# Kernel tuning notes

Measured on AMD Instinct MI355X. Metric: run time of the kernel, lower is better.

## Reference

```python
import math
import jax, jax.numpy as jnp
import numpy as np

T_STEPS = 128       # number of diffusion 'experts'
BASE = 64
CH = BASE * 2       # 128 working channels
TE = 256            # time embedding dim
B, IN_C, H, W = 8, 3, 128, 128
EPS = 1e-5


def _conv(x, w, b):
    # x: [N,C,H,W], w: [O,I,3,3] (or 1x1)
    y = jax.lax.conv_general_dilated(x, w, (1, 1), 'SAME',
                                     dimension_numbers=('NCHW', 'OIHW', 'NCHW'))
    return y + b[None, :, None, None]


def _gn(x, scale, bias, groups=8):
    n, c, h, w = x.shape
    xg = x.reshape(n, groups, c // groups, h, w)
    m = xg.mean((2, 3, 4), keepdims=True)
    v = xg.var((2, 3, 4), keepdims=True)
    xn = ((xg - m) * jax.lax.rsqrt(v + EPS)).reshape(n, c, h, w)
    return xn * scale[None, :, None, None] + bias[None, :, None, None]


def setup_inputs() -> dict:
    key = jax.random.key(0)
    ks = iter(jax.random.split(key, 64))
    def p(shape, s=0.05):
        return jax.random.normal(next(ks), shape, jnp.float32) * s
    return {
        'x': jax.random.normal(next(ks), (B, IN_C, H, W), jnp.float32),
        't': jax.random.randint(next(ks), (B,), 0, T_STEPS),
        # feature_extraction
        'fe_w1': p((BASE, IN_C, 3, 3)), 'fe_b1': jnp.zeros((BASE,), jnp.float32),
        'fe_g1s': jnp.ones((BASE,), jnp.float32), 'fe_g1b': jnp.zeros((BASE,), jnp.float32),
        'fe_w2': p((CH, BASE, 3, 3)), 'fe_b2': jnp.zeros((CH,), jnp.float32),
        'fe_g2s': jnp.ones((CH,), jnp.float32), 'fe_g2b': jnp.zeros((CH,), jnp.float32),
        # stacked per-step expert params [T, ...]
        'mlp_w1': p((T_STEPS, TE, TE)), 'mlp_b1': jnp.zeros((T_STEPS, TE), jnp.float32),
        'mlp_w2': p((T_STEPS, CH, TE)), 'mlp_b2': jnp.zeros((T_STEPS, CH), jnp.float32),
        'c1w': p((T_STEPS, CH, CH + 1, 3, 3)), 'c1b': jnp.zeros((T_STEPS, CH), jnp.float32),
        'g1s': jnp.ones((T_STEPS, CH), jnp.float32), 'g1b': jnp.zeros((T_STEPS, CH), jnp.float32),
        'c2w': p((T_STEPS, CH, CH, 3, 3)), 'c2b': jnp.zeros((T_STEPS, CH), jnp.float32),
        'g2s': jnp.ones((T_STEPS, CH), jnp.float32), 'g2b': jnp.zeros((T_STEPS, CH), jnp.float32),
        'c3w': p((T_STEPS, CH, CH, 3, 3)), 'c3b': jnp.zeros((T_STEPS, CH), jnp.float32),
        # color_reconstruction
        'cr_w1': p((BASE, CH, 3, 3)), 'cr_b1': jnp.zeros((BASE,), jnp.float32),
        'cr_gs': jnp.ones((BASE,), jnp.float32), 'cr_gb': jnp.zeros((BASE,), jnp.float32),
        'cr_w2': p((IN_C, BASE, 3, 3)), 'cr_b2': jnp.zeros((IN_C,), jnp.float32),
        # weight_generator (1x1 conv on pooled features)
        'wg_w': p((1, CH, 1, 1)), 'wg_b': jnp.zeros((1,), jnp.float32),
    }


def _expert(xi, tei, w1, b1, w2, b2, cw1, cb1, gs1, gb1, cw2, cb2, gs2, gb2, cw3, cb3):
    # Single-sample DiffusionStep. xi: [C,H,W], tei: [TE]
    h = jax.nn.silu(w1 @ tei + b1)
    tc = (w2 @ h + b2).mean()  # scalar time channel (fix of original view(-1,1,1,1) bug)
    xb = xi[None]  # [1,C,H,W]
    tmap = jnp.broadcast_to(tc, (1, 1) + xi.shape[1:])
    z = jnp.concatenate([xb, tmap], axis=1)  # [1,C+1,H,W]
    z = jax.nn.silu(_gn(_conv(z, cw1, cb1), gs1, gb1))
    z = jax.nn.silu(_gn(_conv(z, cw2, cb2), gs2, gb2))
    z = _conv(z, cw3, cb3)
    return z[0]


def _forward(x, t, fe_w1, fe_b1, fe_g1s, fe_g1b, fe_w2, fe_b2, fe_g2s, fe_g2b,
             mlp_w1, mlp_b1, mlp_w2, mlp_b2, c1w, c1b, g1s, g1b,
             c2w, c2b, g2s, g2b, c3w, c3b,
             cr_w1, cr_b1, cr_gs, cr_gb, cr_w2, cr_b2, wg_w, wg_b):
    feat = jax.nn.silu(_gn(_conv(x, fe_w1, fe_b1), fe_g1s, fe_g1b))
    feat = jax.nn.silu(_gn(_conv(feat, fe_w2, fe_b2), fe_g2s, fe_g2b))  # [B,CH,H,W]

    # sinusoidal time embedding
    half = TE // 2
    freqs = jnp.exp(jnp.arange(half, dtype=jnp.float32) * (-math.log(10000.0) / (half - 1)))
    e = t.astype(jnp.float32)[:, None] * freqs[None, :]
    temb = jnp.concatenate([jnp.sin(e), jnp.cos(e)], axis=-1)  # [B,TE]

    # Each sample matches exactly one step: gather its expert weights, apply once.
    g = lambda a: jnp.take(a, t, axis=0)
    noise = jax.vmap(_expert)(feat, temb,
                              g(mlp_w1), g(mlp_b1), g(mlp_w2), g(mlp_b2),
                              g(c1w), g(c1b), g(g1s), g(g1b),
                              g(c2w), g(c2b), g(g2s), g(g2b),
                              g(c3w), g(c3b))
    alpha = 1.0 - t.astype(jnp.float32) / T_STEPS
    x_t = feat - alpha[:, None, None, None] * noise

    r = jax.nn.silu(_gn(_conv(x_t, cr_w1, cr_b1), cr_gs, cr_gb))
    restored = jax.nn.sigmoid(_conv(r, cr_w2, cr_b2))  # [B,3,H,W]

    pooled = x_t.mean((2, 3))  # adaptive avg pool to 1x1 -> [B,CH]
    weight = jax.nn.sigmoid(pooled @ wg_w[:, :, 0, 0].T + wg_b)[:, :, None, None]  # [B,1,1,1]
    return restored, weight


def reference(x, t, fe_w1, fe_b1, fe_g1s, fe_g1b, fe_w2, fe_b2, fe_g2s, fe_g2b,
              mlp_w1, mlp_b1, mlp_w2, mlp_b2, c1w, c1b, g1s, g1b,
              c2w, c2b, g2s, g2b, c3w, c3b,
              cr_w1, cr_b1, cr_gs, cr_gb, cr_w2, cr_b2, wg_w, wg_b):
    return _forward(x, t, fe_w1, fe_b1, fe_g1s, fe_g1b, fe_w2, fe_b2, fe_g2s, fe_g2b,
                    mlp_w1, mlp_b1, mlp_w2, mlp_b2, c1w, c1b, g1s, g1b,
                    c2w, c2b, g2s, g2b, c3w, c3b,
                    cr_w1, cr_b1, cr_gs, cr_gb, cr_w2, cr_b2, wg_w, wg_b)
```

## Files before the change

### kernel.cpp

```cpp
#include <hip/hip_runtime.h>
#include <hip/hip_bf16.h>

typedef __hip_bfloat16 bf16;

#define HW 128
#define IMG 16384
#define EPSV 1e-5f

typedef __bf16 b16x8 __attribute__((ext_vector_type(8)));
typedef float f32x16 __attribute__((ext_vector_type(16)));

__device__ __forceinline__ float u2f(unsigned int u){ union{unsigned int i; float f;}c; c.i=u; return c.f; }
__device__ __forceinline__ float blo(unsigned int u){ return u2f(u<<16); }
__device__ __forceinline__ float bhi(unsigned int u){ return u2f(u & 0xffff0000u); }
__device__ __forceinline__ unsigned short f2bu(float v){ bf16 h=__float2bfloat16(v); union{bf16 b; unsigned short s;}c; c.b=h; return c.s; }
__device__ __forceinline__ unsigned int pk(float a, float b){ return (unsigned int)f2bu(a) | ((unsigned int)f2bu(b)<<16); }
__device__ __forceinline__ bf16 f2b(float v){ return __float2bfloat16(v); }
__device__ __forceinline__ float sigm(float x){ return 1.f/(1.f+__expf(-x)); }

__device__ __forceinline__ void gload16(const void* g, void* l) {
    __builtin_amdgcn_global_load_lds((const __attribute__((address_space(1))) unsigned int*)(g),
                                     (__attribute__((address_space(3))) unsigned int*)(l), 16, 0, 0);
}

__device__ __forceinline__ f32x16 MFMA(b16x8 a, b16x8 b, f32x16 c){
    return __builtin_amdgcn_mfma_f32_32x32x16_bf16(a, b, c, 0, 0, 0);
}

template<int CIN, int COUT, bool TADD, bool FUSE_GN, bool FUSE_XT>
__global__ void __launch_bounds__(256, 2)
mfma_conv3x3(const bf16* __restrict__ act,
             const bf16* __restrict__ Wt,
             const float* __restrict__ Bt,
             bf16* __restrict__ outp,
             const float* __restrict__ Tt,
             const bf16* __restrict__ zerobuf,
             float* __restrict__ gpart,
             const bf16* __restrict__ featA,
             const int* __restrict__ tsel,
             const float* __restrict__ wgw,
             float* __restrict__ wpart)
{
    static_assert(CIN==64 || CIN==128, "");
    static_assert(COUT==64 || COUT==128, "");
    constexpr int NT  = COUT/64;
    constexpr int CH  = CIN/64;
    constexpr int P   = 9*CH;
    constexpr int WCH = COUT/8;
    constexpr int WSZ = WCH*1024;

    __shared__ char Xb[33792];
    __shared__ char Wa[2][WSZ];
    __shared__ float redS[4][4], redSS[4][4], redW[4];

    const int n    = blockIdx.z;
    const int tile = blockIdx.x;
    const int y0   = tile*2;
    const int tid  = threadIdx.x;
    const int lane = tid & 63;
    const int wid  = tid >> 6;
    const int wm   = wid >> 1;
    const int wn   = wid & 1;
    const int l31  = lane & 31;
    const int lhi  = lane >> 5;

    const bf16* actN = act + (size_t)n * IMG * CIN;
    const bf16* WtN  = Wt  + (size_t)n * 9 * COUT * CIN;

    f32x16 acc[4][NT];
    #pragma unroll
    for (int i=0;i<4;++i)
        #pragma unroll
        for (int j=0;j<NT;++j)
            #pragma unroll
            for (int k=0;k<16;++k) acc[i][j][k] = 0.f;

    auto stage_X = [&](int dy, int ch) {
        const int ry0 = y0 + dy - 1;
        for (int u = wid; u < 33; u += 4) {
            int s = u*8 + (lane>>3);
            int g = lane & 7;
            int r  = (s >= 130) ? 1 : 0;
            int xp = s - r*130;
            int xx = xp - 1;
            int ry = ry0 + r;
            const void* src = zerobuf;
            if (s < 260 && (unsigned)xx < 128u && (unsigned)ry < 128u)
                src = actN + ((size_t)(ry*128 + xx)*CIN + ch*64 + 8*(g ^ (s&7)));
            gload16(src, Xb + u*1024);
        }
    };
    auto stage_W = [&](int r, int ch, int buf) {
        for (int u = wid; u < WCH; u += 4) {
            int co = u*8 + (lane>>3);
            int g  = lane & 7;
            const void* src = WtN + ((size_t)(r*COUT + co)*CIN + ch*64 + 8*(g ^ (co&7)));
            gload16(src, Wa[buf] + u*1024);
        }
    };

    stage_X(0, 0);
    stage_W(0, 0, 0);
    __syncthreads();

    int buf = 0;
    for (int p = 0; p < P; ++p) {
        const int dx = p % 3;
        const int pc = p / 3;
        const int ch = pc % CH;
        const int dy = pc / CH;
        const bool last = (p+1 == P);

        if (!last) {
            const int pn  = p + 1;
            const int ndx = pn % 3;
            const int npc = pn / 3;
            const int nch = npc % CH;
            const int ndy = npc / CH;
            stage_W(ndy*3 + ndx, nch, buf ^ 1);
        }
        (void)dy; (void)ch;

        __builtin_amdgcn_s_setprio(1);
        #pragma unroll
        for (int s = 0; s < 4; ++s) {
            const int koff = s*32 + lhi*16;
            b16x8 bfr[NT];
            #pragma unroll
            for (int q = 0; q < NT; ++q) {
                int co = wn*32*NT + q*32 + l31;
                bfr[q] = *(const b16x8*)(Wa[buf] + co*128 + (koff ^ ((co&7)<<4)));
            }
            b16x8 afr[4];
            #pragma unroll
            for (int mt = 0; mt < 4; ++mt) {
                int sl = wm*130 + mt*32 + l31 + dx;
                afr[mt] = *(const b16x8*)(Xb + sl*128 + (koff ^ ((sl&7)<<4)));
            }
            #pragma unroll
            for (int mt = 0; mt < 4; ++mt)
                #pragma unroll
                for (int q = 0; q < NT; ++q)
                    acc[mt][q] = MFMA(afr[mt], bfr[q], acc[mt][q]);
        }
        __builtin_amdgcn_s_setprio(0);

        if (!last) {
            if (dx == 2) {
                __syncthreads();
                const int pn  = p + 1;
                const int npc = pn / 3;
                stage_X(npc / CH, npc % CH);
                __syncthreads();
            } else {
                __syncthreads();
            }
        }
        buf ^= 1;
    }

    const float* BtN = Bt + n*COUT;
    const int y = y0 + wm;
    bf16* outRow = outp + ((size_t)n*IMG + (size_t)y*128)*COUT;
    const bf16* featRow = FUSE_XT ? (featA + ((size_t)n*IMG + (size_t)y*128)*COUT) : nullptr;
    float alpha = 0.f;
    if (FUSE_XT) alpha = 1.f - (float)tsel[n] * (1.f/128.f);

    float gs[NT], gss[NT], wsum = 0.f;
    #pragma unroll
    for (int q = 0; q < NT; ++q) { gs[q]=0.f; gss[q]=0.f; }

    #pragma unroll
    for (int q = 0; q < NT; ++q) {
        const int co = wn*32*NT + q*32 + l31;
        const float bv = BtN[co];
        float wg = 0.f;
        if (FUSE_XT) wg = wgw[co];
        float T0=0.f, T1=0.f, T2=0.f;
        if (TADD) {
            int yt = (y==0) ? 0 : (y==127 ? 2 : 1);
            const float* Tp = Tt + (size_t)(n*COUT + co)*9 + yt*3;
            T0 = Tp[0]; T1 = Tp[1]; T2 = Tp[2];
        }
        #pragma unroll
        for (int mt = 0; mt < 4; ++mt) {
            #pragma unroll
            for (int reg = 0; reg < 16; ++reg) {
                const int x = mt*32 + (reg&3) + 8*(reg>>2) + 4*lhi;
                float v = acc[mt][q][reg] + bv;
                if (TADD) v += (x==0) ? T0 : (x==127 ? T2 : T1);
                if (FUSE_GN) { gs[q] += v; gss[q] += v*v; }
                if (FUSE_XT) {
                    float fv = __bfloat162float(featRow[(size_t)x*COUT + co]);
                    float xt = fv - alpha*v;
                    outRow[(size_t)x*COUT + co] = f2b(xt);
                    wsum += xt * wg;
                } else {
                    outRow[(size_t)x*COUT + co] = f2b(v);
                }
            }
        }
    }

    if (FUSE_GN) {
        constexpr int LG = (COUT==128) ? 4 : 3;
        #pragma unroll
        for (int q = 0; q < NT; ++q) {
            float a = gs[q], b = gss[q];
            #pragma unroll
            for (int m = 1; m < (1<<LG); m <<= 1) { a += __shfl_xor(a, m); b += __shfl_xor(b, m); }
            a += __shfl_xor(a, 32); b += __shfl_xor(b, 32);
            const int co = wn*32*NT + q*32 + l31;
            if (lhi == 0 && (l31 & ((1<<LG)-1)) == 0) {
                int j = (co >> LG) & 3;
                redS[wid][j] = a; redSS[wid][j] = b;
            }
        }
        __syncthreads();
        if (tid < 8) {
            int g = tid, wn_ = g>>2, j = g&3;
            float S  = redS[wn_][j]  + redS[2+wn_][j];
            float SS = redSS[wn_][j] + redSS[2+wn_][j];
            gpart[((size_t)(n*64 + tile))*16 + 2*g]     = S;
            gpart[((size_t)(n*64 + tile))*16 + 2*g + 1] = SS;
        }
    }
    if (FUSE_XT) {
        float a = wsum;
        #pragma unroll
        for (int m = 1; m < 64; m <<= 1) a += __shfl_xor(a, m);
        if (lane == 0) redW[wid] = a;
        __syncthreads();
        if (tid == 0) wpart[n*64 + tile] = redW[0]+redW[1]+redW[2]+redW[3];
    }
}

__global__ void __launch_bounds__(256)
wtprep_kernel(const float* __restrict__ w, const float* __restrict__ b,
              const int* __restrict__ t, bf16* __restrict__ Wt, float* __restrict__ Bt,
              int CO, int COsrc, int CIN, int CINW, int gather)
{
    int idx = blockIdx.x*256 + threadIdx.x;
    int total = 8*9*CO*CIN;
    if (idx >= total) return;
    int cin = idx & (CIN-1);
    int tmp = idx / CIN;
    int co  = tmp % CO;
    int tmp2 = tmp / CO;
    int r   = tmp2 % 9;
    int n   = tmp2 / 9;
    int sel = gather ? t[n] : 0;
    float v = 0.f;
    if (co < COsrc) v = w[(((size_t)sel*COsrc + co)*CINW + cin)*9 + r];
    Wt[idx] = f2b(v);
    if (cin==0 && r==0) Bt[n*CO+co] = (co < COsrc) ? b[(size_t)sel*COsrc + co] : 0.f;
}

__global__ void __launch_bounds__(256)
tprep_kernel(const int* __restrict__ t, const float* __restrict__ c1w,
             const float* __restrict__ tc, float* __restrict__ Tt)
{
    int idx = blockIdx.x*256 + threadIdx.x;
    if (idx >= 8*128) return;
    int n = idx >> 7, co = idx & 127;
    const float* wp = c1w + ((size_t)t[n]*128 + co)*129*9 + 128*9;
    float w9[9];
    #pragma unroll
    for (int i=0;i<9;++i) w9[i] = wp[i];
    float tcv = tc[n];
    #pragma unroll
    for (int yt=0; yt<3; ++yt)
        #pragma unroll
        for (int xt=0; xt<3; ++xt) {
            float s = 0.f;
            #pragma unroll
            for (int dy=0; dy<3; ++dy)
                #pragma unroll
                for (int dx=0; dx<3; ++dx) {
                    bool vy = (yt==0) ? (dy>=1) : ((yt==2) ? (dy<=1) : true);
                    bool vx = (xt==0) ? (dx>=1) : ((xt==2) ? (dx<=1) : true);
                    if (vy && vx) s += w9[dy*3+dx];
                }
            Tt[(size_t)idx*9 + yt*3+xt] = tcv*s;
        }
}

__global__ void __launch_bounds__(256)
fe1_kernel(const float* __restrict__ in, const float* __restrict__ w,
           const float* __restrict__ bias, bf16* __restrict__ out)
{
    const int n   = blockIdx.z;
    const int co0 = blockIdx.y * 8;
    const int tx0 = (blockIdx.x & 7) * 16;
    const int ty0 = (blockIdx.x >> 3) * 16;
    const int lx = threadIdx.x & 15, ly = threadIdx.x >> 4;
    __shared__ float tileS[18][19];
    float acc[8];
    #pragma unroll
    for (int i=0;i<8;++i) acc[i] = bias[co0+i];
    const float* inN = in + (size_t)n*3*IMG;
    for (int ci=0; ci<3; ++ci) {
        __syncthreads();
        for (int idx = threadIdx.x; idx < 18*18; idx += 256) {
            int tyy = idx/18, txx = idx - tyy*18;
            int gy = ty0+tyy-1, gx = tx0+txx-1;
            float v = 0.f;
            if ((unsigned)gy < 128u && (unsigned)gx < 128u) v = inN[ci*IMG + gy*128+gx];
            tileS[tyy][txx] = v;
        }
        __syncthreads();
        float v[9];
        #pragma unroll
        for (int ky=0;ky<3;++ky)
            #pragma unroll
            for (int kx=0;kx<3;++kx) v[ky*3+kx] = tileS[ly+ky][lx+kx];
        #pragma unroll
        for (int c=0;c<8;++c) {
            const float* wp = w + ((co0+c)*3 + ci)*9;
            #pragma unroll
            for (int k=0;k<9;++k) acc[c] = fmaf(v[k], wp[k], acc[c]);
        }
    }
    int gy = ty0+ly, gx = tx0+lx;
    uint4 o; o.x = pk(acc[0],acc[1]); o.y = pk(acc[2],acc[3]);
    o.z = pk(acc[4],acc[5]); o.w = pk(acc[6],acc[7]);
    *(uint4*)(out + ((size_t)n*IMG + gy*128+gx)*64 + co0) = o;
}

template<int C>
__global__ void __launch_bounds__(256)
gn_stats_nhwc(const bf16* __restrict__ x, float* __restrict__ partials)
{
    constexpr int L2CPG = (C==128) ? 4 : 3;
    const int chunk = blockIdx.x, n = blockIdx.y;
    const int t = threadIdx.x;
    const uint4* pv = (const uint4*)(x + ((size_t)n*IMG + chunk*256 + t)*C);
    float s[8], ss[8];
    #pragma unroll
    for (int g=0; g<8; ++g) { s[g]=0.f; ss[g]=0.f; }
    #pragma unroll
    for (int v=0; v<C/8; ++v) {
        int g = (v*8) >> L2CPG;
        uint4 u = pv[v];
        float f0=blo(u.x), f1=bhi(u.x), f2=blo(u.y), f3=bhi(u.y);
        float f4=blo(u.z), f5=bhi(u.z), f6=blo(u.w), f7=bhi(u.w);
        s[g]  += ((f0+f1)+(f2+f3)) + ((f4+f5)+(f6+f7));
        ss[g] += ((f0*f0+f1*f1)+(f2*f2+f3*f3)) + ((f4*f4+f5*f5)+(f6*f6+f7*f7));
    }
    __shared__ float sh[16][256];
    #pragma unroll
    for (int g=0; g<8; ++g) { sh[2*g][t] = s[g]; sh[2*g+1][t] = ss[g]; }
    __syncthreads();
    for (int off=128; off>0; off>>=1) {
        if (t < off) {
            #pragma unroll
            for (int k=0;k<16;++k) sh[k][t] += sh[k][t+off];
        }
        __syncthreads();
    }
    if (t < 16) partials[((size_t)n*64 + chunk)*16 + t] = sh[t][0];
}

__global__ void __launch_bounds__(128)
gn_final(const float* __restrict__ partials, const float* __restrict__ scale,
         const float* __restrict__ bias, const int* __restrict__ tsel,
         int C, int l2cpg, float* __restrict__ scA, float* __restrict__ biA)
{
    int n = blockIdx.x, c = threadIdx.x;
    if (c >= C) return;
    int g = c >> l2cpg;
    float s=0.f, ss=0.f;
    for (int k=0;k<64;++k) {
        s  += partials[((size_t)n*64+k)*16 + 2*g];
        ss += partials[((size_t)n*64+k)*16 + 2*g + 1];
    }
    float cnt = (float)IMG * (float)(C>>3);
    float m = s/cnt, var = ss/cnt - m*m;
    float r = rsqrtf(var + EPSV);
    int po = tsel ? tsel[n]*C : 0;
    float sc = scale[po+c]*r;
    scA[n*C+c] = sc;
    biA[n*C+c] = bias[po+c] - m*sc;
}

template<int C>
__global__ void __launch_bounds__(256)
gn_apply_nhwc(bf16* __restrict__ x, const float* __restrict__ scA, const float* __restrict__ biA)
{
    size_t e0 = ((size_t)blockIdx.x*256 + threadIdx.x)*8;
    int n = (int)(e0 >> ((C==128) ? 21 : 20));
    int c0 = (int)(e0 & (C-1));
    const float4 sA = *(const float4*)(scA + n*C + c0);
    const float4 sB = *(const float4*)(scA + n*C + c0 + 4);
    const float4 bA = *(const float4*)(biA + n*C + c0);
    const float4 bB = *(const float4*)(biA + n*C + c0 + 4);
    uint4* p = (uint4*)(x + e0);
    uint4 u = *p;
    float f[8] = {blo(u.x),bhi(u.x),blo(u.y),bhi(u.y),blo(u.z),bhi(u.z),blo(u.w),bhi(u.w)};
    f[0]=f[0]*sA.x+bA.x; f[1]=f[1]*sA.y+bA.y; f[2]=f[2]*sA.z+bA.z; f[3]=f[3]*sA.w+bA.w;
    f[4]=f[4]*sB.x+bB.x; f[5]=f[5]*sB.y+bB.y; f[6]=f[6]*sB.z+bB.z; f[7]=f[7]*sB.w+bB.w;
    #pragma unroll
    for (int i=0;i<8;++i) f[i] = f[i]*sigm(f[i]);
    u.x = pk(f[0],f[1]); u.y = pk(f[2],f[3]); u.z = pk(f[4],f[5]); u.w = pk(f[6],f[7]);
    *p = u;
}

__global__ void __launch_bounds__(256)
time_mlp_kernel(const int* __restrict__ t,
                const float* __restrict__ w1, const float* __restrict__ b1,
                const float* __restrict__ w2, const float* __restrict__ b2,
                float* __restrict__ tc)
{
    const int n = blockIdx.x;
    const int ti = t[n];
    const int tid = threadIdx.x;
    __shared__ float temb[256];
    __shared__ float h[256];
    {
        int j = tid & 127;
        float fr = expf(-9.210340371976184f / 127.f * (float)j);
        float e = (float)ti * fr;
        temb[tid] = (tid < 128) ? sinf(e) : cosf(e);
    }
    __syncthreads();
    {
        const float* w1p = w1 + ((size_t)ti * 256 + tid) * 256;
        float s = b1[(size_t)ti * 256 + tid];
        for (int j = 0; j < 256; ++j) s += w1p[j] * temb[j];
        h[tid] = s * sigm(s);
    }
    __syncthreads();
    float part = 0.f;
    if (tid < 128) {
        const float* w2p = w2 + ((size_t)ti * 128 + tid) * 256;
        float s = b2[(size_t)ti * 128 + tid];
        for (int j = 0; j < 256; ++j) s += w2p[j] * h[j];
        part = s;
    }
    __shared__ float red[256];
    red[tid] = part;
    __syncthreads();
    for (int off = 128; off > 0; off >>= 1) {
        if (tid < off) red[tid] += red[tid + off];
        __syncthreads();
    }
    if (tid == 0) tc[n] = red[0] * (1.f / 128.f);
}

__global__ void __launch_bounds__(64)
weight_final_kernel(const float* __restrict__ wpart, const float* __restrict__ wg_b,
                    float* __restrict__ outw)
{
    const int n = blockIdx.x;
    float s = wpart[n*64 + threadIdx.x];
    #pragma unroll
    for (int m = 1; m < 64; m <<= 1) s += __shfl_xor(s, m);
    if (threadIdx.x == 0) outw[n] = sigm(s * (1.f/16384.f) + wg_b[0]);
}

__global__ void __launch_bounds__(256)
extract_kernel(const bf16* __restrict__ in, float* __restrict__ out)
{
    int n = blockIdx.y;
    int px = blockIdx.x*256 + threadIdx.x;
    const bf16* p = in + ((size_t)n*IMG + px)*64;
    float r0 = __bfloat162float(p[0]);
    float r1 = __bfloat162float(p[1]);
    float r2 = __bfloat162float(p[2]);
    size_t ob = (size_t)n*3*IMG + px;
    out[ob]         = sigm(r0);
    out[ob + IMG]   = sigm(r1);
    out[ob + 2*IMG] = sigm(r2);
}

extern "C" void kernel_launch(void* const* d_in, const int* in_sizes, int n_in,
                              void* d_out, int out_size, void* d_ws, size_t ws_size,
                              hipStream_t stream)
{
    (void)in_sizes; (void)n_in; (void)out_size; (void)ws_size;

    const float* x      = (const float*)d_in[0];
    const int*   t      = (const int*)  d_in[1];
    const float* fe_w1  = (const float*)d_in[2];
    const float* fe_b1  = (const float*)d_in[3];
    const float* fe_g1s = (const float*)d_in[4];
    const float* fe_g1b = (const float*)d_in[5];
    const float* fe_w2  = (const float*)d_in[6];
    const float* fe_b2  = (const float*)d_in[7];
    const float* fe_g2s = (const float*)d_in[8];
    const float* fe_g2b = (const float*)d_in[9];
    const float* mlp_w1 = (const float*)d_in[10];
    const float* mlp_b1 = (const float*)d_in[11];
    const float* mlp_w2 = (const float*)d_in[12];
    const float* mlp_b2 = (const float*)d_in[13];
    const float* c1w    = (const float*)d_in[14];
    const float* c1b    = (const float*)d_in[15];
    const float* g1s    = (const float*)d_in[16];
    const float* g1b    = (const float*)d_in[17];
    const float* c2w    = (const float*)d_in[18];
    const float* c2b    = (const float*)d_in[19];
    const float* g2s    = (const float*)d_in[20];
    const float* g2b    = (const float*)d_in[21];
    const float* c3w    = (const float*)d_in[22];
    const float* c3b    = (const float*)d_in[23];
    const float* cr_w1  = (const float*)d_in[24];
    const float* cr_b1  = (const float*)d_in[25];
    const float* cr_gs  = (const float*)d_in[26];
    const float* cr_gb  = (const float*)d_in[27];
    const float* cr_w2  = (const float*)d_in[28];
    const float* cr_b2  = (const float*)d_in[29];
    const float* wg_w   = (const float*)d_in[30];
    const float* wg_b   = (const float*)d_in[31];

    char* ws = (char*)d_ws;
    bf16* A   = (bf16*)(ws);
    bf16* Bb  = (bf16*)(ws + 33554432);
    bf16* Cb  = (bf16*)(ws + 67108864);
    bf16* Wt  = (bf16*)(ws + 100663296);
    float* Bt = (float*)(ws + 103022592);
    float* Tt = (float*)(ws + 103026688);
    float* tc = (float*)(ws + 103063552);
    bf16* zb  = (bf16*)(ws + 103063616);
    float* gp = (float*)(ws + 103063680);
    float* scA = (float*)(ws + 103096448);
    float* biA = (float*)(ws + 103100544);
    float* wp  = (float*)(ws + 103104640);

    float* out_img = (float*)d_out;
    float* out_w   = out_img + 393216;

    dim3 blk(256);
    dim3 cgrid(64, 1, 8);
    hipMemsetAsync(zb, 0, 64, stream);

    time_mlp_kernel<<<8, blk, 0, stream>>>(t, mlp_w1, mlp_b1, mlp_w2, mlp_b2, tc);
    tprep_kernel<<<4, blk, 0, stream>>>(t, c1w, tc, Tt);

    fe1_kernel<<<dim3(64, 8, 8), blk, 0, stream>>>(x, fe_w1, fe_b1, Bb);
    gn_stats_nhwc<64><<<dim3(64, 8), blk, 0, stream>>>(Bb, gp);
    gn_final<<<8, 128, 0, stream>>>(gp, fe_g1s, fe_g1b, nullptr, 64, 3, scA, biA);
    gn_apply_nhwc<64><<<4096, blk, 0, stream>>>(Bb, scA, biA);

    wtprep_kernel<<<2304, blk, 0, stream>>>(fe_w2, fe_b2, t, Wt, Bt, 128, 128, 64, 64, 0);
    mfma_conv3x3<64,128,false,true,false><<<cgrid, blk, 0, stream>>>(Bb, Wt, Bt, A, nullptr, zb, gp, nullptr, nullptr, nullptr, nullptr);
    gn_final<<<8, 128, 0, stream>>>(gp, fe_g2s, fe_g2b, nullptr, 128, 4, scA, biA);
    gn_apply_nhwc<128><<<8192, blk, 0, stream>>>(A, scA, biA);

    wtprep_kernel<<<4608, blk, 0, stream>>>(c1w, c1b, t, Wt, Bt, 128, 128, 128, 129, 1);
    mfma_conv3x3<128,128,true,true,false><<<cgrid, blk, 0, stream>>>(A, Wt, Bt, Bb, Tt, zb, gp, nullptr, nullptr, nullptr, nullptr);
    gn_final<<<8, 128, 0, stream>>>(gp, g1s, g1b, t, 128, 4, scA, biA);
    gn_apply_nhwc<128><<<8192, blk, 0, stream>>>(Bb, scA, biA);

    wtprep_kernel<<<4608, blk, 0, stream>>>(c2w, c2b, t, Wt, Bt, 128, 128, 128, 128, 1);
    mfma_conv3x3<128,128,false,true,false><<<cgrid, blk, 0, stream>>>(Bb, Wt, Bt, Cb, nullptr, zb, gp, nullptr, nullptr, nullptr, nullptr);
    gn_final<<<8, 128, 0, stream>>>(gp, g2s, g2b, t, 128, 4, scA, biA);
    gn_apply_nhwc<128><<<8192, blk, 0, stream>>>(Cb, scA, biA);

    wtprep_kernel<<<4608, blk, 0, stream>>>(c3w, c3b, t, Wt, Bt, 128, 128, 128, 128, 1);
    mfma_conv3x3<128,128,false,false,true><<<cgrid, blk, 0, stream>>>(Cb, Wt, Bt, Bb, nullptr, zb, nullptr, A, t, wg_w, wp);
    weight_final_kernel<<<8, 64, 0, stream>>>(wp, wg_b, out_w);

    wtprep_kernel<<<2304, blk, 0, stream>>>(cr_w1, cr_b1, t, Wt, Bt, 64, 64, 128, 128, 0);
    mfma_conv3x3<128,64,false,true,false><<<cgrid, blk, 0, stream>>>(Bb, Wt, Bt, Cb, nullptr, zb, gp, nullptr, nullptr, nullptr, nullptr);
    gn_final<<<8, 128, 0, stream>>>(gp, cr_gs, cr_gb, nullptr, 64, 3, scA, biA);
    gn_apply_nhwc<64><<<4096, blk, 0, stream>>>(Cb, scA, biA);

    wtprep_kernel<<<1152, blk, 0, stream>>>(cr_w2, cr_b2, t, Wt, Bt, 64, 3, 64, 64, 0);
    mfma_conv3x3<64,64,false,false,false><<<cgrid, blk, 0, stream>>>(Cb, Wt, Bt, A, nullptr, zb, nullptr, nullptr, nullptr, nullptr, nullptr);
    extract_kernel<<<dim3(64, 8), blk, 0, stream>>>(A, out_img);
}
```

Measured before the change: 375.7 us.

## Use two waves per conv block, each computing all output channels

The conv kernel drops from 4 waves (2x2 split over rows and channels) to 2 waves, one per output row. Each wave now computes every output channel, so its accumulator tile doubles and it reuses each A fragment across all channel tiles. This cuts LDS reads per MFMA but doubles per-thread accumulator registers and halves the threads available for staging and latency hiding. The GroupNorm partial-sum reduction and the weight reduction are rewritten for the new wave layout.

```diff
diff --git a/kernel.cpp b/kernel.cpp
--- a/kernel.cpp
+++ b/kernel.cpp
@@ -28,7 +28,7 @@
 }
 
 template<int CIN, int COUT, bool TADD, bool FUSE_GN, bool FUSE_XT>
-__global__ void __launch_bounds__(256, 2)
+__global__ void __launch_bounds__(128, 1)
 mfma_conv3x3(const bf16* __restrict__ act,
              const bf16* __restrict__ Wt,
              const float* __restrict__ Bt,
@@ -43,7 +43,7 @@
 {
     static_assert(CIN==64 || CIN==128, "");
     static_assert(COUT==64 || COUT==128, "");
-    constexpr int NT  = COUT/64;
+    constexpr int Q   = COUT/32;
     constexpr int CH  = CIN/64;
     constexpr int P   = 9*CH;
     constexpr int WCH = COUT/8;
@@ -51,7 +51,7 @@
 
     __shared__ char Xb[33792];
     __shared__ char Wa[2][WSZ];
-    __shared__ float redS[4][4], redSS[4][4], redW[4];
+    __shared__ float redS[2][8], redSS[2][8], redW[2];
 
     const int n    = blockIdx.z;
     const int tile = blockIdx.x;
@@ -59,25 +59,24 @@
     const int tid  = threadIdx.x;
     const int lane = tid & 63;
     const int wid  = tid >> 6;
-    const int wm   = wid >> 1;
-    const int wn   = wid & 1;
+    const int wm   = wid;
     const int l31  = lane & 31;
     const int lhi  = lane >> 5;
 
     const bf16* actN = act + (size_t)n * IMG * CIN;
     const bf16* WtN  = Wt  + (size_t)n * 9 * COUT * CIN;
 
-    f32x16 acc[4][NT];
+    f32x16 acc[4][Q];
     #pragma unroll
     for (int i=0;i<4;++i)
         #pragma unroll
-        for (int j=0;j<NT;++j)
+        for (int j=0;j<Q;++j)
             #pragma unroll
             for (int k=0;k<16;++k) acc[i][j][k] = 0.f;
 
     auto stage_X = [&](int dy, int ch) {
         const int ry0 = y0 + dy - 1;
-        for (int u = wid; u < 33; u += 4) {
+        for (int u = wid; u < 33; u += 2) {
             int s = u*8 + (lane>>3);
             int g = lane & 7;
             int r  = (s >= 130) ? 1 : 0;
@@ -91,7 +90,7 @@
         }
     };
     auto stage_W = [&](int r, int ch, int buf) {
-        for (int u = wid; u < WCH; u += 4) {
+        for (int u = wid; u < WCH; u += 2) {
             int co = u*8 + (lane>>3);
             int g  = lane & 7;
             const void* src = WtN + ((size_t)(r*COUT + co)*CIN + ch*64 + 8*(g ^ (co&7)));
@@ -106,9 +105,6 @@
     int buf = 0;
     for (int p = 0; p < P; ++p) {
         const int dx = p % 3;
-        const int pc = p / 3;
-        const int ch = pc % CH;
-        const int dy = pc / CH;
         const bool last = (p+1 == P);
 
         if (!last) {
@@ -119,16 +115,15 @@
             const int ndy = npc / CH;
             stage_W(ndy*3 + ndx, nch, buf ^ 1);
         }
-        (void)dy; (void)ch;
 
         __builtin_amdgcn_s_setprio(1);
         #pragma unroll
         for (int s = 0; s < 4; ++s) {
             const int koff = s*32 + lhi*16;
-            b16x8 bfr[NT];
-            #pragma unroll
-            for (int q = 0; q < NT; ++q) {
-                int co = wn*32*NT + q*32 + l31;
+            b16x8 bfr[Q];
+            #pragma unroll
+            for (int q = 0; q < Q; ++q) {
+                int co = q*32 + l31;
                 bfr[q] = *(const b16x8*)(Wa[buf] + co*128 + (koff ^ ((co&7)<<4)));
             }
             b16x8 afr[4];
@@ -140,7 +135,7 @@
             #pragma unroll
             for (int mt = 0; mt < 4; ++mt)
                 #pragma unroll
-                for (int q = 0; q < NT; ++q)
+                for (int q = 0; q < Q; ++q)
                     acc[mt][q] = MFMA(afr[mt], bfr[q], acc[mt][q]);
         }
         __builtin_amdgcn_s_setprio(0);
@@ -166,13 +161,13 @@
     float alpha = 0.f;
     if (FUSE_XT) alpha = 1.f - (float)tsel[n] * (1.f/128.f);
 
-    float gs[NT], gss[NT], wsum = 0.f;
-    #pragma unroll
-    for (int q = 0; q < NT; ++q) { gs[q]=0.f; gss[q]=0.f; }
-
-    #pragma unroll
-    for (int q = 0; q < NT; ++q) {
-        const int co = wn*32*NT + q*32 + l31;
+    float gs[Q], gss[Q], wsum = 0.f;
+    #pragma unroll
+    for (int q = 0; q < Q; ++q) { gs[q]=0.f; gss[q]=0.f; }
+
+    #pragma unroll
+    for (int q = 0; q < Q; ++q) {
+        const int co = q*32 + l31;
         const float bv = BtN[co];
         float wg = 0.f;
         if (FUSE_XT) wg = wgw[co];
@@ -203,26 +198,26 @@
     }
 
     if (FUSE_GN) {
-        constexpr int LG = (COUT==128) ? 4 : 3;
-        #pragma unroll
-        for (int q = 0; q < NT; ++q) {
+        #pragma unroll
+        for (int q = 0; q < Q; ++q) {
             float a = gs[q], b = gss[q];
-            #pragma unroll
-            for (int m = 1; m < (1<<LG); m <<= 1) { a += __shfl_xor(a, m); b += __shfl_xor(b, m); }
-            a += __shfl_xor(a, 32); b += __shfl_xor(b, 32);
-            const int co = wn*32*NT + q*32 + l31;
-            if (lhi == 0 && (l31 & ((1<<LG)-1)) == 0) {
-                int j = (co >> LG) & 3;
-                redS[wid][j] = a; redSS[wid][j] = b;
+            a += __shfl_xor(a,1);  b += __shfl_xor(b,1);
+            a += __shfl_xor(a,2);  b += __shfl_xor(b,2);
+            a += __shfl_xor(a,4);  b += __shfl_xor(b,4);
+            if (COUT == 128) { a += __shfl_xor(a,8); b += __shfl_xor(b,8); }
+            a += __shfl_xor(a,32); b += __shfl_xor(b,32);
+            if (COUT == 128) {
+                if ((lane & 47) == 0) { int j = q*2 + (l31>>4); redS[wid][j] = a; redSS[wid][j] = b; }
+            } else {
+                if ((lane & 39) == 0) { int j = q*4 + (l31>>3); redS[wid][j] = a; redSS[wid][j] = b; }
             }
         }
         __syncthreads();
         if (tid < 8) {
-            int g = tid, wn_ = g>>2, j = g&3;
-            float S  = redS[wn_][j]  + redS[2+wn_][j];
-            float SS = redSS[wn_][j] + redSS[2+wn_][j];
-            gpart[((size_t)(n*64 + tile))*16 + 2*g]     = S;
-            gpart[((size_t)(n*64 + tile))*16 + 2*g + 1] = SS;
+            float S  = redS[0][tid]  + redS[1][tid];
+            float SS = redSS[0][tid] + redSS[1][tid];
+            gpart[((size_t)(n*64 + tile))*16 + 2*tid]     = S;
+            gpart[((size_t)(n*64 + tile))*16 + 2*tid + 1] = SS;
         }
     }
     if (FUSE_XT) {
@@ -231,7 +226,7 @@
         for (int m = 1; m < 64; m <<= 1) a += __shfl_xor(a, m);
         if (lane == 0) redW[wid] = a;
         __syncthreads();
-        if (tid == 0) wpart[n*64 + tile] = redW[0]+redW[1]+redW[2]+redW[3];
+        if (tid == 0) wpart[n*64 + tile] = redW[0] + redW[1];
     }
 }
 
@@ -530,6 +525,7 @@
     float* out_w   = out_img + 393216;
 
     dim3 blk(256);
+    dim3 cblk(128);
     dim3 cgrid(64, 1, 8);
     hipMemsetAsync(zb, 0, 64, stream);
 
@@ -542,30 +538,30 @@
     gn_apply_nhwc<64><<<4096, blk, 0, stream>>>(Bb, scA, biA);
 
     wtprep_kernel<<<2304, blk, 0, stream>>>(fe_w2, fe_b2, t, Wt, Bt, 128, 128, 64, 64, 0);
-    mfma_conv3x3<64,128,false,true,false><<<cgrid, blk, 0, stream>>>(Bb, Wt, Bt, A, nullptr, zb, gp, nullptr, nullptr, nullptr, nullptr);
+    mfma_conv3x3<64,128,false,true,false><<<cgrid, cblk, 0, stream>>>(Bb, Wt, Bt, A, nullptr, zb, gp, nullptr, nullptr, nullptr, nullptr);
     gn_final<<<8, 128, 0, stream>>>(gp, fe_g2s, fe_g2b, nullptr, 128, 4, scA, biA);
     gn_apply_nhwc<128><<<8192, blk, 0, stream>>>(A, scA, biA);
 
     wtprep_kernel<<<4608, blk, 0, stream>>>(c1w, c1b, t, Wt, Bt, 128, 128, 128, 129, 1);
-    mfma_conv3x3<128,128,true,true,false><<<cgrid, blk, 0, stream>>>(A, Wt, Bt, Bb, Tt, zb, gp, nullptr, nullptr, nullptr, nullptr);
+    mfma_conv3x3<128,128,true,true,false><<<cgrid, cblk, 0, stream>>>(A, Wt, Bt, Bb, Tt, zb, gp, nullptr, nullptr, nullptr, nullptr);
     gn_final<<<8, 128, 0, stream>>>(gp, g1s, g1b, t, 128, 4, scA, biA);
     gn_apply_nhwc<128><<<8192, blk, 0, stream>>>(Bb, scA, biA);
 
     wtprep_kernel<<<4608, blk, 0, stream>>>(c2w, c2b, t, Wt, Bt, 128, 128, 128, 128, 1);
-    mfma_conv3x3<128,128,false,true,false><<<cgrid, blk, 0, stream>>>(Bb, Wt, Bt, Cb, nullptr, zb, gp, nullptr, nullptr, nullptr, nullptr);
+    mfma_conv3x3<128,128,false,true,false><<<cgrid, cblk, 0, stream>>>(Bb, Wt, Bt, Cb, nullptr, zb, gp, nullptr, nullptr, nullptr, nullptr);
     gn_final<<<8, 128, 0, stream>>>(gp, g2s, g2b, t, 128, 4, scA, biA);
     gn_apply_nhwc<128><<<8192, blk, 0, stream>>>(Cb, scA, biA);
 
     wtprep_kernel<<<4608, blk, 0, stream>>>(c3w, c3b, t, Wt, Bt, 128, 128, 128, 128, 1);
-    mfma_conv3x3<128,128,false,false,true><<<cgrid, blk, 0, stream>>>(Cb, Wt, Bt, Bb, nullptr, zb, nullptr, A, t, wg_w, wp);
+    mfma_conv3x3<128,128,false,false,true><<<cgrid, cblk, 0, stream>>>(Cb, Wt, Bt, Bb, nullptr, zb, nullptr, A, t, wg_w, wp);
     weight_final_kernel<<<8, 64, 0, stream>>>(wp, wg_b, out_w);
 
     wtprep_kernel<<<2304, blk, 0, stream>>>(cr_w1, cr_b1, t, Wt, Bt, 64, 64, 128, 128, 0);
-    mfma_conv3x3<128,64,false,true,false><<<cgrid, blk, 0, stream>>>(Bb, Wt, Bt, Cb, nullptr, zb, gp, nullptr, nullptr, nullptr, nullptr);
+    mfma_conv3x3<128,64,false,true,false><<<cgrid, cblk, 0, stream>>>(Bb, Wt, Bt, Cb, nullptr, zb, gp, nullptr, nullptr, nullptr, nullptr);
     gn_final<<<8, 128, 0, stream>>>(gp, cr_gs, cr_gb, nullptr, 64, 3, scA, biA);
     gn_apply_nhwc<64><<<4096, blk, 0, stream>>>(Cb, scA, biA);
 
     wtprep_kernel<<<1152, blk, 0, stream>>>(cr_w2, cr_b2, t, Wt, Bt, 64, 3, 64, 64, 0);
-    mfma_conv3x3<64,64,false,false,false><<<cgrid, blk, 0, stream>>>(Cb, Wt, Bt, A, nullptr, zb, nullptr, nullptr, nullptr, nullptr, nullptr);
+    mfma_conv3x3<64,64,false,false,false><<<cgrid, cblk, 0, stream>>>(Cb, Wt, Bt, A, nullptr, zb, nullptr, nullptr, nullptr, nullptr, nullptr);
     extract_kernel<<<dim3(64, 8), blk, 0, stream>>>(A, out_img);
 }
```

New measurement: 722.5 us. +92.3%, slower.

## Read conv weights directly from global and double-buffer input slabs in LDS

Applied to the files above, without the earlier changes.

Removes the LDS staging of weight tiles so each MFMA B-fragment is loaded straight from global memory, with reuse expected to come from cache. The input slab buffer is now double-buffered, so the next slab is prefetched while the current one is computed. This cuts the loop to one barrier per slab instead of one per tap. In exchange, weight fragments become uncoalesced global loads issued inside the MFMA loop, which can add latency, and LDS use grows to two input slabs.

```diff
diff --git a/kernel.cpp b/kernel.cpp
--- a/kernel.cpp
+++ b/kernel.cpp
@@ -43,14 +43,11 @@
 {
     static_assert(CIN==64 || CIN==128, "");
     static_assert(COUT==64 || COUT==128, "");
-    constexpr int NT  = COUT/64;
-    constexpr int CH  = CIN/64;
-    constexpr int P   = 9*CH;
-    constexpr int WCH = COUT/8;
-    constexpr int WSZ = WCH*1024;
-
-    __shared__ char Xb[33792];
-    __shared__ char Wa[2][WSZ];
+    constexpr int NT    = COUT/64;
+    constexpr int CH    = CIN/64;
+    constexpr int NSLAB = 3*CH;
+
+    __shared__ char Xb[2][33792];
     __shared__ float redS[4][4], redSS[4][4], redW[4];
 
     const int n    = blockIdx.z;
@@ -75,7 +72,8 @@
             #pragma unroll
             for (int k=0;k<16;++k) acc[i][j][k] = 0.f;
 
-    auto stage_X = [&](int dy, int ch) {
+    auto stage_X = [&](int slab, int b) {
+        const int dy = slab / CH, ch = slab % CH;
         const int ry0 = y0 + dy - 1;
         for (int u = wid; u < 33; u += 4) {
             int s = u*8 + (lane>>3);
@@ -87,75 +85,49 @@
             const void* src = zerobuf;
             if (s < 260 && (unsigned)xx < 128u && (unsigned)ry < 128u)
                 src = actN + ((size_t)(ry*128 + xx)*CIN + ch*64 + 8*(g ^ (s&7)));
-            gload16(src, Xb + u*1024);
+            gload16(src, Xb[b] + u*1024);
         }
     };
-    auto stage_W = [&](int r, int ch, int buf) {
-        for (int u = wid; u < WCH; u += 4) {
-            int co = u*8 + (lane>>3);
-            int g  = lane & 7;
-            const void* src = WtN + ((size_t)(r*COUT + co)*CIN + ch*64 + 8*(g ^ (co&7)));
-            gload16(src, Wa[buf] + u*1024);
-        }
-    };
 
     stage_X(0, 0);
-    stage_W(0, 0, 0);
     __syncthreads();
 
     int buf = 0;
-    for (int p = 0; p < P; ++p) {
-        const int dx = p % 3;
-        const int pc = p / 3;
-        const int ch = pc % CH;
-        const int dy = pc / CH;
-        const bool last = (p+1 == P);
-
-        if (!last) {
-            const int pn  = p + 1;
-            const int ndx = pn % 3;
-            const int npc = pn / 3;
-            const int nch = npc % CH;
-            const int ndy = npc / CH;
-            stage_W(ndy*3 + ndx, nch, buf ^ 1);
-        }
-        (void)dy; (void)ch;
+    for (int slab = 0; slab < NSLAB; ++slab) {
+        if (slab+1 < NSLAB) stage_X(slab+1, buf^1);
+
+        const int dy = slab / CH, ch = slab % CH;
 
         __builtin_amdgcn_s_setprio(1);
         #pragma unroll
-        for (int s = 0; s < 4; ++s) {
-            const int koff = s*32 + lhi*16;
-            b16x8 bfr[NT];
-            #pragma unroll
-            for (int q = 0; q < NT; ++q) {
-                int co = wn*32*NT + q*32 + l31;
-                bfr[q] = *(const b16x8*)(Wa[buf] + co*128 + (koff ^ ((co&7)<<4)));
+        for (int dx = 0; dx < 3; ++dx) {
+            const int r = dy*3 + dx;
+            const bf16* wtap = WtN + (size_t)(r*COUT)*CIN + ch*64;
+            #pragma unroll
+            for (int s = 0; s < 4; ++s) {
+                const int koff = s*32 + lhi*16;
+                b16x8 bfr[NT];
+                #pragma unroll
+                for (int q = 0; q < NT; ++q) {
+                    int co = wn*32*NT + q*32 + l31;
+                    bfr[q] = *(const b16x8*)(wtap + (size_t)co*CIN + (koff>>1));
+                }
+                b16x8 afr[4];
+                #pragma unroll
+                for (int mt = 0; mt < 4; ++mt) {
+                    int sl = wm*130 + mt*32 + l31 + dx;
+                    afr[mt] = *(const b16x8*)(Xb[buf] + sl*128 + (koff ^ ((sl&7)<<4)));
+                }
+                #pragma unroll
+                for (int mt = 0; mt < 4; ++mt)
+                    #pragma unroll
+                    for (int q = 0; q < NT; ++q)
+                        acc[mt][q] = MFMA(afr[mt], bfr[q], acc[mt][q]);
             }
-            b16x8 afr[4];
-            #pragma unroll
-            for (int mt = 0; mt < 4; ++mt) {
-                int sl = wm*130 + mt*32 + l31 + dx;
-                afr[mt] = *(const b16x8*)(Xb + sl*128 + (koff ^ ((sl&7)<<4)));
-            }
-            #pragma unroll
-            for (int mt = 0; mt < 4; ++mt)
-                #pragma unroll
-                for (int q = 0; q < NT; ++q)
-                    acc[mt][q] = MFMA(afr[mt], bfr[q], acc[mt][q]);
         }
         __builtin_amdgcn_s_setprio(0);
 
-        if (!last) {
-            if (dx == 2) {
-                __syncthreads();
-                const int pn  = p + 1;
-                const int npc = pn / 3;
-                stage_X(npc / CH, npc % CH);
-                __syncthreads();
-            } else {
-                __syncthreads();
-            }
-        }
+        __syncthreads();
         buf ^= 1;
     }
 
```

New measurement: 446.9 us. 1.19x slower.

## Fuse GroupNorm-apply and SiLU into conv input staging, drop standalone apply kernels

Applied to the files above, without the earlier changes.

Removes the separate gn_apply_nhwc passes and instead applies the per-channel GroupNorm scale/bias plus SiLU while staging activation tiles into LDS inside each conv. The feature tensor used for x_t is normalized on the fly in the conv3 epilogue, so each GN layer keeps its own scale/bias buffer. This saves a full read-modify-write of each activation tensor per layer. In exchange, staging now goes through registers with synchronous loads instead of async global_load_lds, and halo pixels get their SiLU recomputed.

```diff
diff --git a/kernel.cpp b/kernel.cpp
--- a/kernel.cpp
+++ b/kernel.cpp
@@ -27,16 +27,19 @@
     return __builtin_amdgcn_mfma_f32_32x32x16_bf16(a, b, c, 0, 0, 0);
 }
 
-template<int CIN, int COUT, bool TADD, bool FUSE_GN, bool FUSE_XT>
+template<int CIN, int COUT, bool TADD, bool GNIN, bool FUSE_GN, bool FUSE_XT>
 __global__ void __launch_bounds__(256, 2)
 mfma_conv3x3(const bf16* __restrict__ act,
              const bf16* __restrict__ Wt,
              const float* __restrict__ Bt,
              bf16* __restrict__ outp,
              const float* __restrict__ Tt,
-             const bf16* __restrict__ zerobuf,
              float* __restrict__ gpart,
+             const float* __restrict__ gnin_sc,
+             const float* __restrict__ gnin_bi,
              const bf16* __restrict__ featA,
+             const float* __restrict__ fsc,
+             const float* __restrict__ fbi,
              const int* __restrict__ tsel,
              const float* __restrict__ wgw,
              float* __restrict__ wpart)
@@ -77,17 +80,34 @@
 
     auto stage_X = [&](int dy, int ch) {
         const int ry0 = y0 + dy - 1;
+        const int g = lane & 7;
+        float sc8[8], bi8[8];
+        if (GNIN) {
+            const float* sp = gnin_sc + n*CIN + ch*64 + g*8;
+            const float* bp = gnin_bi + n*CIN + ch*64 + g*8;
+            #pragma unroll
+            for (int j=0;j<8;++j) { sc8[j]=sp[j]; bi8[j]=bp[j]; }
+        }
         for (int u = wid; u < 33; u += 4) {
-            int s = u*8 + (lane>>3);
-            int g = lane & 7;
+            int s  = u*8 + (lane>>3);
             int r  = (s >= 130) ? 1 : 0;
             int xp = s - r*130;
             int xx = xp - 1;
             int ry = ry0 + r;
-            const void* src = zerobuf;
-            if (s < 260 && (unsigned)xx < 128u && (unsigned)ry < 128u)
-                src = actN + ((size_t)(ry*128 + xx)*CIN + ch*64 + 8*(g ^ (s&7)));
-            gload16(src, Xb + u*1024);
+            uint4 v; v.x=0; v.y=0; v.z=0; v.w=0;
+            bool inb = (s < 260) && ((unsigned)xx < 128u) && ((unsigned)ry < 128u);
+            if (inb) {
+                v = *(const uint4*)(actN + ((size_t)(ry*128 + xx)*CIN + ch*64 + g*8));
+                if (GNIN) {
+                    float f[8] = {blo(v.x),bhi(v.x),blo(v.y),bhi(v.y),
+                                  blo(v.z),bhi(v.z),blo(v.w),bhi(v.w)};
+                    #pragma unroll
+                    for (int j=0;j<8;++j) { float y = f[j]*sc8[j]+bi8[j]; f[j] = y*sigm(y); }
+                    v.x = pk(f[0],f[1]); v.y = pk(f[2],f[3]);
+                    v.z = pk(f[4],f[5]); v.w = pk(f[6],f[7]);
+                }
+            }
+            *(uint4*)(Xb + s*128 + ((g*16) ^ ((s&7)<<4))) = v;
         }
     };
     auto stage_W = [&](int r, int ch, int buf) {
@@ -106,9 +126,6 @@
     int buf = 0;
     for (int p = 0; p < P; ++p) {
         const int dx = p % 3;
-        const int pc = p / 3;
-        const int ch = pc % CH;
-        const int dy = pc / CH;
         const bool last = (p+1 == P);
 
         if (!last) {
@@ -119,7 +136,6 @@
             const int ndy = npc / CH;
             stage_W(ndy*3 + ndx, nch, buf ^ 1);
         }
-        (void)dy; (void)ch;
 
         __builtin_amdgcn_s_setprio(1);
         #pragma unroll
@@ -174,8 +190,12 @@
     for (int q = 0; q < NT; ++q) {
         const int co = wn*32*NT + q*32 + l31;
         const float bv = BtN[co];
-        float wg = 0.f;
-        if (FUSE_XT) wg = wgw[co];
+        float wg = 0.f, fscv = 0.f, fbiv = 0.f;
+        if (FUSE_XT) {
+            wg   = wgw[co];
+            fscv = fsc[n*COUT + co];
+            fbiv = fbi[n*COUT + co];
+        }
         float T0=0.f, T1=0.f, T2=0.f;
         if (TADD) {
             int yt = (y==0) ? 0 : (y==127 ? 2 : 1);
@@ -192,7 +212,9 @@
                 if (FUSE_GN) { gs[q] += v; gss[q] += v*v; }
                 if (FUSE_XT) {
                     float fv = __bfloat162float(featRow[(size_t)x*COUT + co]);
-                    float xt = fv - alpha*v;
+                    float yy = fv*fscv + fbiv;
+                    float feat = yy * sigm(yy);
+                    float xt = feat - alpha*v;
                     outRow[(size_t)x*COUT + co] = f2b(xt);
                     wsum += xt * wg;
                 } else {
@@ -381,28 +403,6 @@
     float sc = scale[po+c]*r;
     scA[n*C+c] = sc;
     biA[n*C+c] = bias[po+c] - m*sc;
-}
-
-template<int C>
-__global__ void __launch_bounds__(256)
-gn_apply_nhwc(bf16* __restrict__ x, const float* __restrict__ scA, const float* __restrict__ biA)
-{
-    size_t e0 = ((size_t)blockIdx.x*256 + threadIdx.x)*8;
-    int n = (int)(e0 >> ((C==128) ? 21 : 20));
-    int c0 = (int)(e0 & (C-1));
-    const float4 sA = *(const float4*)(scA + n*C + c0);
-    const float4 sB = *(const float4*)(scA + n*C + c0 + 4);
-    const float4 bA = *(const float4*)(biA + n*C + c0);
-    const float4 bB = *(const float4*)(biA + n*C + c0 + 4);
-    uint4* p = (uint4*)(x + e0);
-    uint4 u = *p;
-    float f[8] = {blo(u.x),bhi(u.x),blo(u.y),bhi(u.y),blo(u.z),bhi(u.z),blo(u.w),bhi(u.w)};
-    f[0]=f[0]*sA.x+bA.x; f[1]=f[1]*sA.y+bA.y; f[2]=f[2]*sA.z+bA.z; f[3]=f[3]*sA.w+bA.w;
-    f[4]=f[4]*sB.x+bB.x; f[5]=f[5]*sB.y+bB.y; f[6]=f[6]*sB.z+bB.z; f[7]=f[7]*sB.w+bB.w;
-    #pragma unroll
-    for (int i=0;i<8;++i) f[i] = f[i]*sigm(f[i]);
-    u.x = pk(f[0],f[1]); u.y = pk(f[2],f[3]); u.z = pk(f[4],f[5]); u.w = pk(f[6],f[7]);
-    *p = u;
 }
 
 __global__ void __launch_bounds__(256)
@@ -520,52 +520,54 @@
     float* Bt = (float*)(ws + 103022592);
     float* Tt = (float*)(ws + 103026688);
     float* tc = (float*)(ws + 103063552);
-    bf16* zb  = (bf16*)(ws + 103063616);
     float* gp = (float*)(ws + 103063680);
-    float* scA = (float*)(ws + 103096448);
-    float* biA = (float*)(ws + 103100544);
-    float* wp  = (float*)(ws + 103104640);
+    float* wp = (float*)(ws + 103096448);
+    float* scF1 = (float*)(ws + 103098496); float* biF1 = (float*)(ws + 103102592);
+    float* scF2 = (float*)(ws + 103106688); float* biF2 = (float*)(ws + 103110784);
+    float* scC1 = (float*)(ws + 103114880); float* biC1 = (float*)(ws + 103118976);
+    float* scC2 = (float*)(ws + 103123072); float* biC2 = (float*)(ws + 103127168);
+    float* scR1 = (float*)(ws + 103131264); float* biR1 = (float*)(ws + 103135360);
 
     float* out_img = (float*)d_out;
     float* out_w   = out_img + 393216;
 
     dim3 blk(256);
     dim3 cgrid(64, 1, 8);
-    hipMemsetAsync(zb, 0, 64, stream);
 
     time_mlp_kernel<<<8, blk, 0, stream>>>(t, mlp_w1, mlp_b1, mlp_w2, mlp_b2, tc);
     tprep_kernel<<<4, blk, 0, stream>>>(t, c1w, tc, Tt);
 
     fe1_kernel<<<dim3(64, 8, 8), blk, 0, stream>>>(x, fe_w1, fe_b1, Bb);
     gn_stats_nhwc<64><<<dim3(64, 8), blk, 0, stream>>>(Bb, gp);
-    gn_final<<<8, 128, 0, stream>>>(gp, fe_g1s, fe_g1b, nullptr, 64, 3, scA, biA);
-    gn_apply_nhwc<64><<<4096, blk, 0, stream>>>(Bb, scA, biA);
+    gn_final<<<8, 128, 0, stream>>>(gp, fe_g1s, fe_g1b, nullptr, 64, 3, scF1, biF1);
 
     wtprep_kernel<<<2304, blk, 0, stream>>>(fe_w2, fe_b2, t, Wt, Bt, 128, 128, 64, 64, 0);
-    mfma_conv3x3<64,128,false,true,false><<<cgrid, blk, 0, stream>>>(Bb, Wt, Bt, A, nullptr, zb, gp, nullptr, nullptr, nullptr, nullptr);
-    gn_final<<<8, 128, 0, stream>>>(gp, fe_g2s, fe_g2b, nullptr, 128, 4, scA, biA);
-    gn_apply_nhwc<128><<<8192, blk, 0, stream>>>(A, scA, biA);
+    mfma_conv3x3<64,128,false,true,true,false><<<cgrid, blk, 0, stream>>>(
+        Bb, Wt, Bt, A, nullptr, gp, scF1, biF1, nullptr, nullptr, nullptr, nullptr, nullptr, nullptr);
+    gn_final<<<8, 128, 0, stream>>>(gp, fe_g2s, fe_g2b, nullptr, 128, 4, scF2, biF2);
 
     wtprep_kernel<<<4608, blk, 0, stream>>>(c1w, c1b, t, Wt, Bt, 128, 128, 128, 129, 1);
-    mfma_conv3x3<128,128,true,true,false><<<cgrid, blk, 0, stream>>>(A, Wt, Bt, Bb, Tt, zb, gp, nullptr, nullptr, nullptr, nullptr);
-    gn_final<<<8, 128, 0, stream>>>(gp, g1s, g1b, t, 128, 4, scA, biA);
-    gn_apply_nhwc<128><<<8192, blk, 0, stream>>>(Bb, scA, biA);
+    mfma_conv3x3<128,128,true,true,true,false><<<cgrid, blk, 0, stream>>>(
+        A, Wt, Bt, Bb, Tt, gp, scF2, biF2, nullptr, nullptr, nullptr, nullptr, nullptr, nullptr);
+    gn_final<<<8, 128, 0, stream>>>(gp, g1s, g1b, t, 128, 4, scC1, biC1);
 
     wtprep_kernel<<<4608, blk, 0, stream>>>(c2w, c2b, t, Wt, Bt, 128, 128, 128, 128, 1);
-    mfma_conv3x3<128,128,false,true,false><<<cgrid, blk, 0, stream>>>(Bb, Wt, Bt, Cb, nullptr, zb, gp, nullptr, nullptr, nullptr, nullptr);
-    gn_final<<<8, 128, 0, stream>>>(gp, g2s, g2b, t, 128, 4, scA, biA);
-    gn_apply_nhwc<128><<<8192, blk, 0, stream>>>(Cb, scA, biA);
+    mfma_conv3x3<128,128,false,true,true,false><<<cgrid, blk, 0, stream>>>(
+        Bb, Wt, Bt, Cb, nullptr, gp, scC1, biC1, nullptr, nullptr, nullptr, nullptr, nullptr, nullptr);
+    gn_final<<<8, 128, 0, stream>>>(gp, g2s, g2b, t, 128, 4, scC2, biC2);
 
     wtprep_kernel<<<4608, blk, 0, stream>>>(c3w, c3b, t, Wt, Bt, 128, 128, 128, 128, 1);
-    mfma_conv3x3<128,128,false,false,true><<<cgrid, blk, 0, stream>>>(Cb, Wt, Bt, Bb, nullptr, zb, nullptr, A, t, wg_w, wp);
+    mfma_conv3x3<128,128,false,true,false,true><<<cgrid, blk, 0, stream>>>(
+        Cb, Wt, Bt, Bb, nullptr, nullptr, scC2, biC2, A, scF2, biF2, t, wg_w, wp);
     weight_final_kernel<<<8, 64, 0, stream>>>(wp, wg_b, out_w);
 
     wtprep_kernel<<<2304, blk, 0, stream>>>(cr_w1, cr_b1, t, Wt, Bt, 64, 64, 128, 128, 0);
-    mfma_conv3x3<128,64,false,true,false><<<cgrid, blk, 0, stream>>>(Bb, Wt, Bt, Cb, nullptr, zb, gp, nullptr, nullptr, nullptr, nullptr);
-    gn_final<<<8, 128, 0, stream>>>(gp, cr_gs, cr_gb, nullptr, 64, 3, scA, biA);
-    gn_apply_nhwc<64><<<4096, blk, 0, stream>>>(Cb, scA, biA);
+    mfma_conv3x3<128,64,false,false,true,false><<<cgrid, blk, 0, stream>>>(
+        Bb, Wt, Bt, Cb, nullptr, gp, nullptr, nullptr, nullptr, nullptr, nullptr, nullptr, nullptr, nullptr);
+    gn_final<<<8, 128, 0, stream>>>(gp, cr_gs, cr_gb, nullptr, 64, 3, scR1, biR1);
 
     wtprep_kernel<<<1152, blk, 0, stream>>>(cr_w2, cr_b2, t, Wt, Bt, 64, 3, 64, 64, 0);
-    mfma_conv3x3<64,64,false,false,false><<<cgrid, blk, 0, stream>>>(Cb, Wt, Bt, A, nullptr, zb, nullptr, nullptr, nullptr, nullptr, nullptr);
+    mfma_conv3x3<64,64,false,true,false,false><<<cgrid, blk, 0, stream>>>(
+        Cb, Wt, Bt, A, nullptr, nullptr, scR1, biR1, nullptr, nullptr, nullptr, nullptr, nullptr, nullptr);
     extract_kernel<<<dim3(64, 8), blk, 0, stream>>>(A, out_img);
 }
```

New measurement: 468.4 us. 24.7% more time.
